# Performance work log

Hardware: AMD Instinct MI355X
Metric: run time of the kernel (lower is better)

The kernel has to match this reference:

```python
import jax, jax.numpy as jnp
import numpy as np
from jax import lax

D_MODEL = 2048
D_STATE = 16
D_CONV = 4
B_SZ = 2
T_LEN = 2048


def setup_inputs() -> dict:
    key = jax.random.key(0)
    ks = jax.random.split(key, 8)
    x = jax.random.normal(ks[0], (B_SZ, T_LEN, D_MODEL), dtype=jnp.float32)
    h = jnp.zeros((B_SZ, D_MODEL, D_STATE), dtype=jnp.float32)
    norm_w = jnp.ones((D_MODEL,), dtype=jnp.float32)
    in_proj_w = jax.random.normal(ks[1], (2 * D_MODEL, D_MODEL), dtype=jnp.float32) * (D_MODEL ** -0.5)
    conv_w = jax.random.normal(ks[2], (D_MODEL, 1, D_CONV), dtype=jnp.float32) * 0.5
    conv_b = jnp.zeros((D_MODEL,), dtype=jnp.float32)
    x_proj_w = jax.random.normal(ks[3], (D_MODEL + 2 * D_STATE, D_MODEL), dtype=jnp.float32) * (D_MODEL ** -0.5)
    A_log = jnp.broadcast_to(jnp.log(jnp.arange(1, D_STATE + 1, dtype=jnp.float32))[None, :], (D_MODEL, D_STATE)).copy()
    D = jnp.ones((D_MODEL,), dtype=jnp.float32)
    out_proj_w = jax.random.normal(ks[4], (D_MODEL, D_MODEL), dtype=jnp.float32) * (D_MODEL ** -0.5)
    return {"x": x, "h": h, "norm_w": norm_w, "in_proj_w": in_proj_w,
            "conv_w": conv_w, "conv_b": conv_b, "x_proj_w": x_proj_w,
            "A_log": A_log, "D": D, "out_proj_w": out_proj_w}


def _rmsnorm(x, w, eps=1e-6):
    ms = jnp.mean(jnp.square(x.astype(jnp.float32)), axis=-1, keepdims=True)
    return (x * lax.rsqrt(ms + eps).astype(x.dtype)) * w.astype(x.dtype)


def reference(x, h, norm_w, in_proj_w, conv_w, conv_b, x_proj_w, A_log, D, out_proj_w):
    B, T, d_model = x.shape
    d_state = A_log.shape[1]
    residual = x
    x_normed = _rmsnorm(x, norm_w)
    xz = x_normed @ in_proj_w.T                      # (B, T, 2*d_model)
    x_branch, z = jnp.split(xz, 2, axis=-1)
    # depthwise causal conv1d: torch pads both sides by d_conv-1 then slices [:T],
    # equivalent to left-pad-only causal conv.
    xc = x_branch.transpose(0, 2, 1)                 # (B, d_model, T)
    xc = lax.conv_general_dilated(
        xc, conv_w, window_strides=(1,), padding=[(D_CONV - 1, 0)],
        dimension_numbers=("NCH", "OIH", "NCH"), feature_group_count=d_model)
    xc = xc + conv_b[None, :, None]
    x_ssm = jax.nn.silu(xc.transpose(0, 2, 1))       # (B, T, d_model)

    # SSM core
    proj = x_ssm @ x_proj_w.T                        # (B, T, d_model + 2*d_state)
    delta_raw = proj[..., :d_model]
    B_in = proj[..., d_model:d_model + d_state]
    C_in = proj[..., d_model + d_state:]
    delta = jax.nn.softplus(delta_raw)               # (B, T, d_model)
    A = -jnp.exp(A_log.astype(jnp.float32))          # (d_model, d_state)

    def step(h_c, inp):
        d_t, b_t, c_t, x_t = inp                     # (B,dm) (B,ds) (B,ds) (B,dm)
        A_bar = jnp.exp(d_t[:, :, None] * A[None])   # (B, dm, ds)
        h_c = A_bar * h_c + (d_t * x_t)[:, :, None] * b_t[:, None, :]
        y_t = jnp.einsum("bdn,bn->bd", h_c, c_t) + D * x_t
        return h_c, y_t

    xs = (delta.transpose(1, 0, 2), B_in.transpose(1, 0, 2),
          C_in.transpose(1, 0, 2), x_ssm.transpose(1, 0, 2))
    h_new, ys = lax.scan(step, h.astype(x.dtype), xs)
    y = ys.transpose(1, 0, 2)                        # (B, T, d_model)

    y = y * jax.nn.silu(z)
    out = residual + y @ out_proj_w.T
    return out, lax.stop_gradient(h_new)
```

## Files before the change

kernel.cpp:

```cpp
#include <hip/hip_runtime.h>
#include <cstdint>
#include <cstddef>


typedef __bf16 bf16_t;
typedef __attribute__((ext_vector_type(8))) __bf16 bf16x8;
typedef __attribute__((ext_vector_type(4))) __bf16 bf16x4;
typedef __attribute__((ext_vector_type(4))) float f32x4;

#define D_MODEL 2048
#define D_STATE 16
#define B_SZ 2
#define T_LEN 2048
#define N_ROWS (B_SZ * T_LEN)
#define N_PAD  2304
#define N_CHUNK 32
#define L_CHUNK (T_LEN / N_CHUNK)
#define LOG2E 1.4426950408889634f

__device__ __forceinline__ void load_lds16(const void* g, void* l) {
    __builtin_amdgcn_global_load_lds(
        (const __attribute__((address_space(1))) void*)(uintptr_t)g,
        (__attribute__((address_space(3))) void*)(uintptr_t)l,
        16, 0, 0);
}

#define VMW(n) asm volatile("s_waitcnt vmcnt(" #n ")" ::: "memory")
#define BARP() __builtin_amdgcn_s_barrier()
#define BARG() do { __builtin_amdgcn_s_barrier(); __builtin_amdgcn_sched_barrier(0); } while (0)

__global__ __launch_bounds__(256) void cast_w13(
    const float* __restrict__ w1, const float* __restrict__ w3,
    bf16_t* __restrict__ d1, bf16_t* __restrict__ d3)
{
    int i = blockIdx.x * 256 + threadIdx.x;
    const int n1 = 4096 * 2048 / 4;
    if (i < n1) {
        f32x4 v = ((const f32x4*)w1)[i];
        ((bf16x4*)d1)[i] = __builtin_convertvector(v, bf16x4);
    } else {
        int j = i - n1;
        f32x4 v = ((const f32x4*)w3)[j];
        ((bf16x4*)d3)[j] = __builtin_convertvector(v, bf16x4);
    }
}

__global__ __launch_bounds__(256) void cast_pad_w2(
    const float* __restrict__ s, bf16_t* __restrict__ d)
{
    int i = blockIdx.x * 256 + threadIdx.x;
    int row = i >> 11;
    int col = i & 2047;
    float v = (row < 2080) ? s[(size_t)row * 2048 + col] : 0.f;
    d[i] = (bf16_t)v;
}

__global__ __launch_bounds__(256) void rmsnorm_kernel(
    const float* __restrict__ x, const float* __restrict__ w,
    bf16_t* __restrict__ xn)
{
    int row = blockIdx.x;
    int tid = threadIdx.x;
    const f32x4* xr = (const f32x4*)(x + (size_t)row * D_MODEL);
    f32x4 v0 = xr[tid];
    f32x4 v1 = xr[tid + 256];
    float ss = 0.f;
    #pragma unroll
    for (int e = 0; e < 4; ++e) { ss = fmaf(v0[e], v0[e], ss); ss = fmaf(v1[e], v1[e], ss); }
    #pragma unroll
    for (int o = 32; o > 0; o >>= 1) ss += __shfl_down(ss, o, 64);
    __shared__ float red[4];
    if ((tid & 63) == 0) red[tid >> 6] = ss;
    __syncthreads();
    float tot = red[0] + red[1] + red[2] + red[3];
    float scale = rsqrtf(tot * (1.f / D_MODEL) + 1e-6f);
    const f32x4* w4 = (const f32x4*)w;
    f32x4 m0 = v0 * w4[tid] * scale;
    f32x4 m1 = v1 * w4[tid + 256] * scale;
    bf16x4* xo = (bf16x4*)(xn + (size_t)row * D_MODEL);
    xo[tid]       = __builtin_convertvector(m0, bf16x4);
    xo[tid + 256] = __builtin_convertvector(m1, bf16x4);
}

template<int MODE>
__global__ __launch_bounds__(512, 2) void gemm_bt(
    const bf16_t* __restrict__ A, const bf16_t* __restrict__ Bw, int K,
    float* __restrict__ out0, bf16_t* __restrict__ out1,
    const float* __restrict__ add)
{
    __shared__ __align__(16) char smem[131072];
    char* const ldsAp = smem;
    char* const ldsBp = smem + 32768;

    const int tid  = threadIdx.x;
    const int nwg = gridDim.x * gridDim.y;
    const int lin = blockIdx.x + gridDim.x * blockIdx.y;
    const int wg  = (lin & 7) * (nwg >> 3) + (lin >> 3);
    const int bm  = wg & 15;
    const int bn  = wg >> 4;

    const int lane = tid & 63;
    const int wave = tid >> 6;
    const int wm   = wave >> 2;
    const int wn   = wave & 3;
    const int fr   = lane & 15;
    const int quad = lane >> 4;

    const int rS   = tid >> 2;
    const int cS   = tid & 3;
    const int gcol = ((cS - ((rS >> 1) & 3)) & 3) * 8;
    const bf16_t* sAn = A  + (size_t)(bm * 256 + rS) * K + gcol;
    const bf16_t* sBn = Bw + (size_t)(bn * 256 + rS) * K + gcol;

    const int swz  = ((quad + ((fr >> 1) & 3)) & 3) * 8;
    const int aOff = (wm * 128 + fr) * 32 + swz;
    const int bOff = (wn * 64  + fr) * 32 + swz;

    f32x4 acc[8][4];
    #pragma unroll
    for (int i = 0; i < 8; ++i)
        #pragma unroll
        for (int j = 0; j < 4; ++j) acc[i][j] = {0.f, 0.f, 0.f, 0.f};

    bf16x8 bfr[4];

#define STG_A(b, s) do { \
        char* l_ = ldsAp + (b) * 65536 + (s) * 16384 + tid * 16; \
        load_lds16(sAn, l_); load_lds16(sAn + (size_t)128 * K, l_ + 8192); \
        sAn += 32; } while (0)
#define STG_B(b, s) do { \
        char* l_ = ldsBp + (b) * 65536 + (s) * 16384 + tid * 16; \
        load_lds16(sBn, l_); load_lds16(sBn + (size_t)128 * K, l_ + 8192); \
        sBn += 32; } while (0)

#define PHASE(BUF, S, IH, STAGE_STMT, TAIL_STMT, CLOSE)                       \
    {                                                                         \
        const bf16_t* pA_ = (const bf16_t*)(ldsAp + (BUF)*65536 + (S)*16384); \
        if ((IH) == 0) {                                                      \
            const bf16_t* pB_ =                                               \
                (const bf16_t*)(ldsBp + (BUF)*65536 + (S)*16384);             \
            _Pragma("unroll")                                                 \
            for (int j = 0; j < 4; ++j)                                       \
                bfr[j] = *(const bf16x8*)(pB_ + bOff + j * 512);              \
        }                                                                     \
        bf16x8 af0 = *(const bf16x8*)(pA_ + aOff + ((IH)*4 + 0) * 512);       \
        bf16x8 af1 = *(const bf16x8*)(pA_ + aOff + ((IH)*4 + 1) * 512);       \
        bf16x8 af2 = *(const bf16x8*)(pA_ + aOff + ((IH)*4 + 2) * 512);       \
        bf16x8 af3 = *(const bf16x8*)(pA_ + aOff + ((IH)*4 + 3) * 512);       \
        STAGE_STMT;                                                           \
        BARP();                                                               \
        __builtin_amdgcn_s_setprio(1);                                        \
        _Pragma("unroll")                                                     \
        for (int j = 0; j < 4; ++j)                                           \
            acc[(IH)*4+0][j] = __builtin_amdgcn_mfma_f32_16x16x32_bf16(       \
                af0, bfr[j], acc[(IH)*4+0][j], 0, 0, 0);                      \
        _Pragma("unroll")                                                     \
        for (int j = 0; j < 4; ++j)                                           \
            acc[(IH)*4+1][j] = __builtin_amdgcn_mfma_f32_16x16x32_bf16(       \
                af1, bfr[j], acc[(IH)*4+1][j], 0, 0, 0);                      \
        _Pragma("unroll")                                                     \
        for (int j = 0; j < 4; ++j)                                           \
            acc[(IH)*4+2][j] = __builtin_amdgcn_mfma_f32_16x16x32_bf16(       \
                af2, bfr[j], acc[(IH)*4+2][j], 0, 0, 0);                      \
        _Pragma("unroll")                                                     \
        for (int j = 0; j < 4; ++j)                                           \
            acc[(IH)*4+3][j] = __builtin_amdgcn_mfma_f32_16x16x32_bf16(       \
                af3, bfr[j], acc[(IH)*4+3][j], 0, 0, 0);                      \
        __builtin_amdgcn_s_setprio(0);                                        \
        TAIL_STMT;                                                            \
        CLOSE();                                                              \
    }

    STG_B(0, 0); STG_A(0, 0); STG_B(0, 1); STG_A(0, 1);
    STG_B(1, 0); STG_A(1, 0); STG_B(1, 1);
    VMW(6); BARG();

    const int NI = K >> 7;
    for (int I = 0; I < NI - 1; ++I) {
        PHASE(0, 0, 0, STG_A(1, 1), (void)0, BARP)
        PHASE(0, 0, 1, STG_B(0, 0), (void)0, BARP)
        PHASE(0, 1, 0, STG_A(0, 0), (void)0, BARP)
        PHASE(0, 1, 1, STG_B(0, 1), VMW(6),  BARG)
        PHASE(1, 0, 0, STG_A(0, 1), (void)0, BARP)
        PHASE(1, 0, 1, STG_B(1, 0), (void)0, BARP)
        PHASE(1, 1, 0, STG_A(1, 0), (void)0, BARP)
        PHASE(1, 1, 1, STG_B(1, 1), VMW(6),  BARG)
    }
    PHASE(0, 0, 0, STG_A(1, 1), (void)0, BARP)
    PHASE(0, 0, 1, (void)0,     (void)0, BARP)
    PHASE(0, 1, 0, (void)0,     (void)0, BARP)
    PHASE(0, 1, 1, (void)0,     VMW(0),  BARG)
    PHASE(1, 0, 0, (void)0,     (void)0, BARP)
    PHASE(1, 0, 1, (void)0,     (void)0, BARP)
    PHASE(1, 1, 0, (void)0,     (void)0, BARP)
    PHASE(1, 1, 1, (void)0,     (void)0, BARP)
#undef STG_A
#undef STG_B
#undef PHASE

    float* const cs = (float*)smem;
    __syncthreads();
    #pragma unroll
    for (int s = 0; s < 4; ++s) {
        if (wm == (s >> 1)) {
            #pragma unroll
            for (int ii = 0; ii < 4; ++ii)
                #pragma unroll
                for (int j = 0; j < 4; ++j)
                    #pragma unroll
                    for (int rr = 0; rr < 4; ++rr)
                        cs[(ii * 16 + quad * 4 + rr) * 268 + wn * 64 + j * 16 + fr]
                            = acc[(s & 1) * 4 + ii][j][rr];
        }
        __syncthreads();
        #pragma unroll
        for (int k = 0; k < 8; ++k) {
            const int idx = tid + k * 512;
            const int row = idx >> 6;
            const int c4  = (idx & 63) << 2;
            f32x4 v = *(const f32x4*)(cs + row * 268 + c4);
            const int gr = bm * 256 + s * 64 + row;
            const int gc = bn * 256 + c4;
            if (MODE == 0) {
                if (bn < 8) {
                    *(f32x4*)&out0[(size_t)gr * 2048 + gc] = v;
                } else {
                    bf16x4 o;
                    #pragma unroll
                    for (int e = 0; e < 4; ++e) {
                        float sv = v[e];
                        o[e] = (bf16_t)(sv / (1.f + __expf(-sv)));
                    }
                    *(bf16x4*)&out1[(size_t)gr * 2048 + (gc - 2048)] = o;
                }
            } else if (MODE == 1) {
                if (bn < 8) {
                    #pragma unroll
                    for (int e = 0; e < 4; ++e) {
                        float sv = v[e];
                        v[e] = fmaxf(sv, 0.f) + __logf(1.f + __expf(-fabsf(sv)));
                    }
                }
                *(f32x4*)&out0[(size_t)gr * N_PAD + gc] = v;
            } else {
                f32x4 a4 = *(const f32x4*)&add[(size_t)gr * 2048 + gc];
                *(f32x4*)&out0[(size_t)gr * 2048 + gc] = v + a4;
            }
        }
        __syncthreads();
    }
}

__global__ __launch_bounds__(256) void conv_silu_kernel(
    const float* __restrict__ xb, const float* __restrict__ cw,
    const float* __restrict__ cb, bf16_t* __restrict__ xs_b)
{
    int id = blockIdx.x * 256 + threadIdx.x;
    int d  = id & 2047;
    int tb = (id >> 11) & 255;
    int b  = id >> 19;
    float w0 = cw[d * 4 + 0], w1 = cw[d * 4 + 1], w2 = cw[d * 4 + 2], w3 = cw[d * 4 + 3];
    float bias = cb[d];
    int t0 = tb * 8;
    size_t base = (size_t)b * T_LEN;
    float v[11];
    #pragma unroll
    for (int i = 0; i < 11; ++i) {
        int t = t0 - 3 + i;
        v[i] = (t >= 0) ? xb[(base + t) * 2048 + d] : 0.f;
    }
    #pragma unroll
    for (int j = 0; j < 8; ++j) {
        float s = bias + w0 * v[j] + w1 * v[j + 1] + w2 * v[j + 2] + w3 * v[j + 3];
        float sl = s / (1.f + __expf(-s));
        xs_b[(base + t0 + j) * D_MODEL + d] = (bf16_t)sl;
    }
}

#define PF 4

__global__ __launch_bounds__(256) void scan_phase1(
    const float* __restrict__ proj, const bf16_t* __restrict__ xs,
    const float* __restrict__ A_log,
    float* __restrict__ Aprod, float* __restrict__ hfin)
{
    int wi   = blockIdx.x * 4 + (threadIdx.x >> 6);
    int lane = threadIdx.x & 63;
    int nq   = lane & 3;
    int dsub = lane >> 2;
    int c  = wi & 31;
    int dg = (wi >> 5) & 127;
    int b  = wi >> 12;
    int dd = dg * 16 + dsub;

    float A2[4], h[4], Ap[4];
    #pragma unroll
    for (int j = 0; j < 4; ++j) {
        A2[j] = -__expf(A_log[dd * D_STATE + nq * 4 + j]) * LOG2E;
        h[j] = 0.f; Ap[j] = 1.f;
    }
    const int t0 = c * L_CHUNK;
    const int tmax = t0 + L_CHUNK - 1;

    float p_da[PF], p_xv[PF];
    f32x4 p_B[PF];
    #pragma unroll
    for (int u = 0; u < PF; ++u) {
        size_t row = (size_t)b * T_LEN + t0 + u;
        const float* pr = proj + row * N_PAD;
        p_da[u] = pr[dd];
        p_xv[u] = (float)xs[row * D_MODEL + dd];
        p_B[u]  = *(const f32x4*)(pr + D_MODEL + nq * 4);
    }

    for (int it = 0; it < L_CHUNK; it += PF) {
        #pragma unroll
        for (int u = 0; u < PF; ++u) {
            int t = t0 + it + u;
            float da = p_da[u], xv = p_xv[u];
            f32x4 Bv = p_B[u];
            int tn = t + PF; tn = (tn > tmax) ? tmax : tn;
            {
                size_t row = (size_t)b * T_LEN + tn;
                const float* pr = proj + row * N_PAD;
                p_da[u] = pr[dd];
                p_xv[u] = (float)xs[row * D_MODEL + dd];
                p_B[u]  = *(const f32x4*)(pr + D_MODEL + nq * 4);
            }
            float dx = da * xv;
            #pragma unroll
            for (int j = 0; j < 4; ++j) {
                float a = exp2f(da * A2[j]);
                Ap[j] *= a;
                h[j] = fmaf(a, h[j], dx * Bv[j]);
            }
        }
    }
    size_t o = ((size_t)c * 4096 + b * 2048 + dd) * D_STATE + nq * 4;
    *(f32x4*)(Aprod + o) = f32x4{Ap[0], Ap[1], Ap[2], Ap[3]};
    *(f32x4*)(hfin  + o) = f32x4{h[0], h[1], h[2], h[3]};
}

__global__ __launch_bounds__(256) void scan_phase2(
    const float* __restrict__ h_in, const float* __restrict__ Aprod,
    float* __restrict__ hfin, float* __restrict__ h_out)
{
    int g = blockIdx.x * 256 + threadIdx.x;
    float h = h_in[g];
    for (int c = 0; c < N_CHUNK; ++c) {
        size_t o = (size_t)c * 65536 + g;
        float a   = Aprod[o];
        float loc = hfin[o];
        hfin[o] = h;
        h = fmaf(a, h, loc);
    }
    h_out[g] = h;
}

__global__ __launch_bounds__(256) void scan_phase3(
    const float* __restrict__ proj, const bf16_t* __restrict__ xs,
    const bf16_t* __restrict__ zg, const float* __restrict__ A_log,
    const float* __restrict__ Dv, const float* __restrict__ hinit,
    bf16_t* __restrict__ yg)
{
    int wi   = blockIdx.x * 4 + (threadIdx.x >> 6);
    int lane = threadIdx.x & 63;
    int nq   = lane & 3;
    int dsub = lane >> 2;
    int c  = wi & 31;
    int dg = (wi >> 5) & 127;
    int b  = wi >> 12;
    int dd = dg * 16 + dsub;

    float A2[4], h[4];
    size_t o = ((size_t)c * 4096 + b * 2048 + dd) * D_STATE + nq * 4;
    #pragma unroll
    for (int j = 0; j < 4; ++j) {
        A2[j] = -__expf(A_log[dd * D_STATE + nq * 4 + j]) * LOG2E;
        h[j]  = hinit[o + j];
    }
    float Dd = Dv[dd];
    const int t0 = c * L_CHUNK;
    const int tmax = t0 + L_CHUNK - 1;

    float p_da[PF], p_xv[PF], p_sz[PF];
    f32x4 p_B[PF], p_C[PF];
    #pragma unroll
    for (int u = 0; u < PF; ++u) {
        size_t row = (size_t)b * T_LEN + t0 + u;
        const float* pr = proj + row * N_PAD;
        p_da[u] = pr[dd];
        p_xv[u] = (float)xs[row * D_MODEL + dd];
        p_sz[u] = (float)zg[row * 2048 + dd];
        p_B[u]  = *(const f32x4*)(pr + D_MODEL + nq * 4);
        p_C[u]  = *(const f32x4*)(pr + D_MODEL + D_STATE + nq * 4);
    }

    for (int it = 0; it < L_CHUNK; it += PF) {
        #pragma unroll
        for (int u = 0; u < PF; ++u) {
            int t = t0 + it + u;
            float da = p_da[u], xv = p_xv[u], sz = p_sz[u];
            f32x4 Bv = p_B[u], Cv = p_C[u];
            int tn = t + PF; tn = (tn > tmax) ? tmax : tn;
            {
                size_t row = (size_t)b * T_LEN + tn;
                const float* pr = proj + row * N_PAD;
                p_da[u] = pr[dd];
                p_xv[u] = (float)xs[row * D_MODEL + dd];
                p_sz[u] = (float)zg[row * 2048 + dd];
                p_B[u]  = *(const f32x4*)(pr + D_MODEL + nq * 4);
                p_C[u]  = *(const f32x4*)(pr + D_MODEL + D_STATE + nq * 4);
            }
            float dx = da * xv;
            float yp = 0.f;
            #pragma unroll
            for (int j = 0; j < 4; ++j) {
                float a = exp2f(da * A2[j]);
                h[j] = fmaf(a, h[j], dx * Bv[j]);
                yp = fmaf(h[j], Cv[j], yp);
            }
            yp += __shfl_xor(yp, 1, 64);
            yp += __shfl_xor(yp, 2, 64);
            if (nq == 0) {
                float y = fmaf(Dd, xv, yp);
                yg[((size_t)b * T_LEN + t) * D_MODEL + dd] = (bf16_t)(y * sz);
            }
        }
    }
}

extern "C" void kernel_launch(void* const* d_in, const int* in_sizes, int n_in,
                              void* d_out, int out_size, void* d_ws, size_t ws_size,
                              hipStream_t stream)
{
    const float* x    = (const float*)d_in[0];
    const float* h0   = (const float*)d_in[1];
    const float* nw   = (const float*)d_in[2];
    const float* w_in = (const float*)d_in[3];
    const float* cw   = (const float*)d_in[4];
    const float* cb   = (const float*)d_in[5];
    const float* w_x  = (const float*)d_in[6];
    const float* alog = (const float*)d_in[7];
    const float* dv   = (const float*)d_in[8];
    const float* w_out= (const float*)d_in[9];
    float* out  = (float*)d_out;
    float* hout = out + (size_t)N_ROWS * D_MODEL;

    char* ws = (char*)d_ws;
    size_t off = 0;
    auto alloc = [&](size_t bytes) -> void* {
        void* p = ws + off;
        off += (bytes + 255) & ~(size_t)255;
        return p;
    };
    bf16_t* W1  = (bf16_t*)alloc((size_t)4096 * 2048 * 2);
    bf16_t* W2  = (bf16_t*)alloc((size_t)N_PAD * 2048 * 2);
    bf16_t* W3  = (bf16_t*)alloc((size_t)2048 * 2048 * 2);
    bf16_t* XN  = (bf16_t*)alloc((size_t)N_ROWS * 2048 * 2);
    float*  XB  = (float*) alloc((size_t)N_ROWS * 2048 * 4);
    bf16_t* ZG  = (bf16_t*)alloc((size_t)N_ROWS * 2048 * 2);
    float*  PROJ= (float*) alloc((size_t)N_ROWS * N_PAD * 4);
    float* APROD= (float*) alloc((size_t)N_CHUNK * 4096 * D_STATE * 4);
    float* HFIN = (float*) alloc((size_t)N_CHUNK * 4096 * D_STATE * 4);
    bf16_t* XSb = W1;
    bf16_t* YG  = XN;

    cast_w13<<<(4096 * 2048 / 4 + 2048 * 2048 / 4) / 256, 256, 0, stream>>>(w_in, w_out, W1, W3);
    cast_pad_w2<<<(N_PAD * 2048) / 256, 256, 0, stream>>>(w_x, W2);

    rmsnorm_kernel<<<N_ROWS, 256, 0, stream>>>(x, nw, XN);
    gemm_bt<0><<<dim3(16, 16), 512, 0, stream>>>(XN, W1, 2048, XB, ZG, nullptr);
    conv_silu_kernel<<<(B_SZ * (T_LEN / 8) * D_MODEL) / 256, 256, 0, stream>>>(XB, cw, cb, XSb);
    gemm_bt<1><<<dim3(16, N_PAD / 256), 512, 0, stream>>>(XSb, W2, 2048, PROJ, nullptr, nullptr);
    scan_phase1<<<2048, 256, 0, stream>>>(PROJ, XSb, alog, APROD, HFIN);
    scan_phase2<<<256, 256, 0, stream>>>(h0, APROD, HFIN, hout);
    scan_phase3<<<2048, 256, 0, stream>>>(PROJ, XSb, ZG, alog, dv, HFIN, YG);
    gemm_bt<2><<<dim3(16, 8), 512, 0, stream>>>(YG, W3, 2048, out, nullptr, x);

    (void)in_sizes; (void)n_in; (void)out_size; (void)ws_size;
}
```

Measured before the change: 475.9 us.

## Double-buffer LDS fragment registers to overlap LDS reads with MFMA in GEMM

Restructures the GEMM main loop so the A/B fragments for the next phase are read from LDS into a second register set while the current phase's MFMAs issue, instead of reading then computing serially. Each phase now issues its MFMAs first, then global-to-LDS staging and next-fragment LDS reads, followed by a single barrier per phase, with vmcnt waits adjusted. This aims to hide LDS latency behind matrix-core work, at the cost of more VGPRs and a more delicate barrier/wait ordering that could introduce hazards.

```diff
diff --git a/kernel.cpp b/kernel.cpp
--- a/kernel.cpp
+++ b/kernel.cpp
@@ -26,7 +26,6 @@
 }
 
 #define VMW(n) asm volatile("s_waitcnt vmcnt(" #n ")" ::: "memory")
-#define BARP() __builtin_amdgcn_s_barrier()
 #define BARG() do { __builtin_amdgcn_s_barrier(); __builtin_amdgcn_sched_barrier(0); } while (0)
 
 __global__ __launch_bounds__(256) void cast_w13(
@@ -122,7 +121,8 @@
         #pragma unroll
         for (int j = 0; j < 4; ++j) acc[i][j] = {0.f, 0.f, 0.f, 0.f};
 
-    bf16x8 bfr[4];
+    bf16x8 afr[2][4];
+    bf16x8 bfr[2][4];
 
 #define STG_A(b, s) do { \
         char* l_ = ldsAp + (b) * 65536 + (s) * 16384 + tid * 16; \
@@ -133,70 +133,57 @@
         load_lds16(sBn, l_); load_lds16(sBn + (size_t)128 * K, l_ + 8192); \
         sBn += 32; } while (0)
 
-#define PHASE(BUF, S, IH, STAGE_STMT, TAIL_STMT, CLOSE)                       \
-    {                                                                         \
-        const bf16_t* pA_ = (const bf16_t*)(ldsAp + (BUF)*65536 + (S)*16384); \
-        if ((IH) == 0) {                                                      \
-            const bf16_t* pB_ =                                               \
-                (const bf16_t*)(ldsBp + (BUF)*65536 + (S)*16384);             \
-            _Pragma("unroll")                                                 \
-            for (int j = 0; j < 4; ++j)                                       \
-                bfr[j] = *(const bf16x8*)(pB_ + bOff + j * 512);              \
-        }                                                                     \
-        bf16x8 af0 = *(const bf16x8*)(pA_ + aOff + ((IH)*4 + 0) * 512);       \
-        bf16x8 af1 = *(const bf16x8*)(pA_ + aOff + ((IH)*4 + 1) * 512);       \
-        bf16x8 af2 = *(const bf16x8*)(pA_ + aOff + ((IH)*4 + 2) * 512);       \
-        bf16x8 af3 = *(const bf16x8*)(pA_ + aOff + ((IH)*4 + 3) * 512);       \
-        STAGE_STMT;                                                           \
-        BARP();                                                               \
-        __builtin_amdgcn_s_setprio(1);                                        \
+#define MFMA16(MIH, MAB, MBB)                                                 \
+    __builtin_amdgcn_s_setprio(1);                                            \
+    _Pragma("unroll")                                                         \
+    for (int i = 0; i < 4; ++i)                                               \
         _Pragma("unroll")                                                     \
         for (int j = 0; j < 4; ++j)                                           \
-            acc[(IH)*4+0][j] = __builtin_amdgcn_mfma_f32_16x16x32_bf16(       \
-                af0, bfr[j], acc[(IH)*4+0][j], 0, 0, 0);                      \
-        _Pragma("unroll")                                                     \
-        for (int j = 0; j < 4; ++j)                                           \
-            acc[(IH)*4+1][j] = __builtin_amdgcn_mfma_f32_16x16x32_bf16(       \
-                af1, bfr[j], acc[(IH)*4+1][j], 0, 0, 0);                      \
-        _Pragma("unroll")                                                     \
-        for (int j = 0; j < 4; ++j)                                           \
-            acc[(IH)*4+2][j] = __builtin_amdgcn_mfma_f32_16x16x32_bf16(       \
-                af2, bfr[j], acc[(IH)*4+2][j], 0, 0, 0);                      \
-        _Pragma("unroll")                                                     \
-        for (int j = 0; j < 4; ++j)                                           \
-            acc[(IH)*4+3][j] = __builtin_amdgcn_mfma_f32_16x16x32_bf16(       \
-                af3, bfr[j], acc[(IH)*4+3][j], 0, 0, 0);                      \
-        __builtin_amdgcn_s_setprio(0);                                        \
-        TAIL_STMT;                                                            \
-        CLOSE();                                                              \
-    }
+            acc[(MIH)*4+i][j] = __builtin_amdgcn_mfma_f32_16x16x32_bf16(      \
+                afr[MAB][i], bfr[MBB][j], acc[(MIH)*4+i][j], 0, 0, 0);        \
+    __builtin_amdgcn_s_setprio(0);
+
+#define RD_A(RBUF, RS, RIH, RAB) {                                            \
+    const bf16_t* pA_ = (const bf16_t*)(ldsAp + (RBUF)*65536 + (RS)*16384);   \
+    _Pragma("unroll")                                                         \
+    for (int i = 0; i < 4; ++i)                                               \
+        afr[RAB][i] = *(const bf16x8*)(pA_ + aOff + ((RIH)*4+i)*512); }
+
+#define RD_B(RBUF, RS, RBB) {                                                 \
+    const bf16_t* pB_ = (const bf16_t*)(ldsBp + (RBUF)*65536 + (RS)*16384);   \
+    _Pragma("unroll")                                                         \
+    for (int j = 0; j < 4; ++j)                                               \
+        bfr[RBB][j] = *(const bf16x8*)(pB_ + bOff + j*512); }
 
     STG_B(0, 0); STG_A(0, 0); STG_B(0, 1); STG_A(0, 1);
     STG_B(1, 0); STG_A(1, 0); STG_B(1, 1);
     VMW(6); BARG();
+    RD_B(0, 0, 0) RD_A(0, 0, 0, 0)
 
     const int NI = K >> 7;
     for (int I = 0; I < NI - 1; ++I) {
-        PHASE(0, 0, 0, STG_A(1, 1), (void)0, BARP)
-        PHASE(0, 0, 1, STG_B(0, 0), (void)0, BARP)
-        PHASE(0, 1, 0, STG_A(0, 0), (void)0, BARP)
-        PHASE(0, 1, 1, STG_B(0, 1), VMW(6),  BARG)
-        PHASE(1, 0, 0, STG_A(0, 1), (void)0, BARP)
-        PHASE(1, 0, 1, STG_B(1, 0), (void)0, BARP)
-        PHASE(1, 1, 0, STG_A(1, 0), (void)0, BARP)
-        PHASE(1, 1, 1, STG_B(1, 1), VMW(6),  BARG)
-    }
-    PHASE(0, 0, 0, STG_A(1, 1), (void)0, BARP)
-    PHASE(0, 0, 1, (void)0,     (void)0, BARP)
-    PHASE(0, 1, 0, (void)0,     (void)0, BARP)
-    PHASE(0, 1, 1, (void)0,     VMW(0),  BARG)
-    PHASE(1, 0, 0, (void)0,     (void)0, BARP)
-    PHASE(1, 0, 1, (void)0,     (void)0, BARP)
-    PHASE(1, 1, 0, (void)0,     (void)0, BARP)
-    PHASE(1, 1, 1, (void)0,     (void)0, BARP)
+        MFMA16(0,0,0) STG_A(1,1); RD_A(0,0,1,1)                  BARG();
+        MFMA16(1,1,0) STG_B(0,0); RD_B(0,1,1) RD_A(0,1,0,0) VMW(4); BARG();
+        MFMA16(0,0,1) STG_A(0,0); RD_A(0,1,1,1)                  BARG();
+        MFMA16(1,1,1) STG_B(0,1); RD_B(1,0,0) RD_A(1,0,0,0) VMW(4); BARG();
+        MFMA16(0,0,0) STG_A(0,1); RD_A(1,0,1,1)                  BARG();
+        MFMA16(1,1,0) STG_B(1,0); RD_B(1,1,1) RD_A(1,1,0,0) VMW(4); BARG();
+        MFMA16(0,0,1) STG_A(1,0); RD_A(1,1,1,1)                  BARG();
+        MFMA16(1,1,1) STG_B(1,1); RD_B(0,0,0) RD_A(0,0,0,0) VMW(4); BARG();
+    }
+    MFMA16(0,0,0) STG_A(1,1); RD_A(0,0,1,1)              BARG();
+    MFMA16(1,1,0) RD_B(0,1,1) RD_A(0,1,0,0)      VMW(4); BARG();
+    MFMA16(0,0,1) RD_A(0,1,1,1)                          BARG();
+    MFMA16(1,1,1) RD_B(1,0,0) RD_A(1,0,0,0)      VMW(0); BARG();
+    MFMA16(0,0,0) RD_A(1,0,1,1)                          BARG();
+    MFMA16(1,1,0) RD_B(1,1,1) RD_A(1,1,0,0)              BARG();
+    MFMA16(0,0,1) RD_A(1,1,1,1)                          BARG();
+    MFMA16(1,1,1)
 #undef STG_A
 #undef STG_B
-#undef PHASE
+#undef MFMA16
+#undef RD_A
+#undef RD_B
 
     float* const cs = (float*)smem;
     __syncthreads();
```

New measurement: 471.2 us. About the same (-1.0%).
